# Performance work log

Measured on AMD Instinct MI355X. Metric: run time of the kernel, lower is better.

## Reference

```python
import jax, jax.numpy as jnp
import numpy as np


def setup_inputs() -> dict:
    key = jax.random.key(0)
    k1, k2, k3, k4 = jax.random.split(key, 4)
    B, S, H, P = 8, 2048, 1024, 4096
    hidden_states = jax.random.normal(k1, (B, S, H), dtype=jnp.float32)
    pairs = jax.random.randint(k2, (B, P, 2), 0, S, dtype=jnp.int64)
    # classifier params: Linear(2H -> H), Linear(H -> 2). Stored as (in, out).
    W1 = jax.random.normal(k3, (2 * H, H), dtype=jnp.float32) * (1.0 / np.sqrt(2 * H))
    b1 = jnp.zeros((H,), dtype=jnp.float32)
    W2 = jax.random.normal(k4, (H, 2), dtype=jnp.float32) * (1.0 / np.sqrt(H))
    b2 = jnp.zeros((2,), dtype=jnp.float32)
    return {"hidden_states": hidden_states, "pairs": pairs,
            "W1": W1, "b1": b1, "W2": W2, "b2": b2}


def reference(hidden_states, pairs, W1, b1, W2, b2):
    # Gather pair embeddings: (B, P, H) each.
    emb1 = jnp.take_along_axis(hidden_states, pairs[:, :, 0:1], axis=1)
    emb2 = jnp.take_along_axis(hidden_states, pairs[:, :, 1:2], axis=1)
    pair_emb = jnp.concatenate([emb1, emb2], axis=-1)  # (B, P, 2H)
    h = jnp.einsum('bpi,ih->bph', pair_emb, W1) + b1
    h = jax.nn.gelu(h, approximate=False)  # torch nn.GELU default is exact erf
    # Dropout is identity at inference.
    logits = jnp.einsum('bph,ho->bpo', h, W2) + b2  # (B, P, 2)
    return logits
```

## Files before the change

### kernel.cpp

```cpp
#include <hip/hip_runtime.h>
#include <hip/hip_bf16.h>

#define B_  8
#define S_  2048
#define H_  1024
#define P_  4096
#define K_  2048
#define M_  32768

typedef unsigned short u16;
using bf16x8 = __attribute__((ext_vector_type(8))) short;
using f32x4  = __attribute__((ext_vector_type(4))) float;

__device__ inline u16 f2bf(float f) {
  union { float f; unsigned u; } c; c.f = f;
  unsigned u = c.u;
  unsigned r = (u + 0x7fffu + ((u >> 16) & 1u)) >> 16;
  return (u16)r;
}

__global__ void cvt_hidden_k(const float4* __restrict__ src,
                             ushort4* __restrict__ dst, int n4) {
  int i = blockIdx.x * blockDim.x + threadIdx.x;
  int stride = gridDim.x * blockDim.x;
  for (; i < n4; i += stride) {
    float4 v = src[i];
    ushort4 o;
    o.x = f2bf(v.x); o.y = f2bf(v.y); o.z = f2bf(v.z); o.w = f2bf(v.w);
    dst[i] = o;
  }
}

__global__ void transp_w1_k(const float* __restrict__ w1, u16* __restrict__ w1t) {
  __shared__ float tile[32][33];
  int n0 = blockIdx.x * 32;
  int k0 = blockIdx.y * 32;
  int tx = threadIdx.x;
  int ty = threadIdx.y;
#pragma unroll
  for (int i = 0; i < 32; i += 8)
    tile[ty + i][tx] = w1[(size_t)(k0 + ty + i) * H_ + n0 + tx];
  __syncthreads();
#pragma unroll
  for (int i = 0; i < 32; i += 8)
    w1t[(size_t)(n0 + ty + i) * K_ + k0 + tx] = f2bf(tile[tx][ty + i]);
}

__global__ __launch_bounds__(512, 2) void gemm_k(
    const u16*  __restrict__ hidB,
    const u16*  __restrict__ w1t,
    const int*  __restrict__ pairs,
    const float* __restrict__ b1,
    const float2* __restrict__ w2,
    float*      __restrict__ part)
{
  __shared__ u16 ldsA[2][256 * 64];
  __shared__ u16 ldsB[2][256 * 64];

  int orig = blockIdx.x;
  int bid = (orig & 7) * (512 >> 3) + (orig >> 3);
  int nt = bid & 3;
  int mt = bid >> 2;
  int n0 = nt * 256;
  int m0 = mt * 256;
  int bI = m0 >> 12;
  int pp = m0 & 4095;

  int t = threadIdx.x;
  int w = t >> 6;
  int l = t & 63;
  int lr = l & 15;
  int lj = l >> 4;
  int wr = w >> 2;
  int wn = w & 3;

  int2 sv[4];
#pragma unroll
  for (int it = 0; it < 4; ++it) {
    int r = it * 64 + w * 8 + (l >> 3);
    sv[it] = ((const int2*)pairs)[bI * P_ + pp + r];
  }

  const u16* hidBase = hidB + ((size_t)bI << 21);

  f32x4 acc[8][4];
#pragma unroll
  for (int i = 0; i < 8; ++i)
#pragma unroll
    for (int j = 0; j < 4; ++j)
      acc[i][j] = (f32x4){0.f, 0.f, 0.f, 0.f};

  auto STAGE = [&](int buf, int kt) {
    int k0 = kt * 64;
    int kcol = k0 & 1023;
    int half = k0 >> 10;
#pragma unroll
    for (int it = 0; it < 4; ++it) {
      int r  = it * 64 + w * 8 + (l >> 3);
      int gs = (l & 7) ^ (r & 7);
      int s  = half ? sv[it].y : sv[it].x;
      __builtin_amdgcn_global_load_lds(
          (const __attribute__((address_space(1))) void*)
              (hidBase + (((size_t)s) << 10) + kcol + gs * 8),
          (__attribute__((address_space(3))) void*)&ldsA[buf][(it * 64 + w * 8) * 64],
          16, 0, 0);
      __builtin_amdgcn_global_load_lds(
          (const __attribute__((address_space(1))) void*)
              (w1t + ((size_t)(n0 + r)) * K_ + k0 + gs * 8),
          (__attribute__((address_space(3))) void*)&ldsB[buf][(it * 64 + w * 8) * 64],
          16, 0, 0);
    }
  };

  STAGE(0, 0);
  __syncthreads();

  int cur = 0;
  for (int kt = 0; kt < K_ / 64; ++kt) {
    if (kt < K_ / 64 - 1) STAGE(cur ^ 1, kt + 1);

#pragma unroll
    for (int ks = 0; ks < 2; ++ks) {
      bf16x8 af[8], bv[4];
      int gw = ks * 4 + lj;
#pragma unroll
      for (int mi = 0; mi < 8; ++mi) {
        int row = wr * 128 + mi * 16 + lr;
        af[mi] = *(const bf16x8*)&ldsA[cur][row * 64 + ((gw ^ (row & 7)) * 8)];
      }
#pragma unroll
      for (int ni = 0; ni < 4; ++ni) {
        int row = wn * 64 + ni * 16 + lr;
        bv[ni] = *(const bf16x8*)&ldsB[cur][row * 64 + ((gw ^ (row & 7)) * 8)];
      }
#pragma unroll
      for (int mi = 0; mi < 8; ++mi)
#pragma unroll
        for (int ni = 0; ni < 4; ++ni)
          acc[mi][ni] = __builtin_amdgcn_mfma_f32_16x16x32_bf16(
              af[mi], bv[ni], acc[mi][ni], 0, 0, 0);
    }
    __syncthreads();
    cur ^= 1;
  }

  int q = nt * 4 + wn;
  float2* pOut = (float2*)part;
#pragma unroll
  for (int mi = 0; mi < 8; ++mi) {
    float s0[4] = {0.f, 0.f, 0.f, 0.f};
    float s1[4] = {0.f, 0.f, 0.f, 0.f};
#pragma unroll
    for (int ni = 0; ni < 4; ++ni) {
      int n = n0 + wn * 64 + ni * 16 + lr;
      float bb = b1[n];
      float2 wv = w2[n];
#pragma unroll
      for (int j = 0; j < 4; ++j) {
        float x = acc[mi][ni][j] + bb;
        float g = 0.5f * x * (1.0f + erff(x * 0.70710678118654752f));
        s0[j] += g * wv.x;
        s1[j] += g * wv.y;
      }
    }
#pragma unroll
    for (int off = 1; off < 16; off <<= 1) {
#pragma unroll
      for (int j = 0; j < 4; ++j) {
        s0[j] += __shfl_xor(s0[j], off, 64);
        s1[j] += __shfl_xor(s1[j], off, 64);
      }
    }
    if (lr == 0) {
#pragma unroll
      for (int j = 0; j < 4; ++j) {
        int m = m0 + wr * 128 + mi * 16 + lj * 4 + j;
        pOut[((size_t)q << 15) + m] = make_float2(s0[j], s1[j]);
      }
    }
  }
}

__global__ void reduce_k(const float2* __restrict__ part,
                         const float* __restrict__ b2,
                         float2* __restrict__ out) {
  int m = blockIdx.x * blockDim.x + threadIdx.x;
  if (m >= M_) return;
  float a0 = b2[0], a1 = b2[1];
#pragma unroll
  for (int q = 0; q < 16; ++q) {
    float2 v = part[((size_t)q << 15) + m];
    a0 += v.x; a1 += v.y;
  }
  out[m] = make_float2(a0, a1);
}

extern "C" void kernel_launch(void* const* d_in, const int* in_sizes, int n_in,
                              void* d_out, int out_size, void* d_ws, size_t ws_size,
                              hipStream_t stream) {
  const float* hidden = (const float*)d_in[0];
  const int*   pairs  = (const int*)d_in[1];
  const float* W1     = (const float*)d_in[2];
  const float* b1     = (const float*)d_in[3];
  const float* W2     = (const float*)d_in[4];
  const float* b2     = (const float*)d_in[5];
  float* out = (float*)d_out;

  u16* hidB = (u16*)d_ws;
  u16* w1t  = hidB + (size_t)B_ * S_ * H_;
  float* part = (float*)(w1t + (size_t)H_ * K_);

  int n4 = (B_ * S_ * H_) / 4;
  cvt_hidden_k<<<4096, 256, 0, stream>>>((const float4*)hidden, (ushort4*)hidB, n4);
  transp_w1_k<<<dim3(H_ / 32, K_ / 32), dim3(32, 8), 0, stream>>>(W1, w1t);
  gemm_k<<<(M_ / 256) * (H_ / 256), 512, 0, stream>>>(
      hidB, w1t, pairs, b1, (const float2*)W2, part);
  reduce_k<<<(M_ + 255) / 256, 256, 0, stream>>>(
      (const float2*)part, b2, (float2*)out);
}
```

Baseline: 200.3 us.

## Deepen GEMM K-pipeline to four stages with explicit vmcnt waits and setprio

Restructures the GEMM main loop from a double-buffered 64-wide K tile into a four-buffer, 32-wide K tile pipeline with three stages in flight. It uses manual s_waitcnt vmcnt counters and raw s_barrier instead of __syncthreads, and raises wave priority around the MFMA block. The aim is to hide global-to-LDS load latency behind compute and cut barrier overhead. The cost is twice as many loop iterations and barriers, plus fragile hand-counted waits that must exactly match the outstanding loads.

```diff
diff --git a/kernel.cpp b/kernel.cpp
--- a/kernel.cpp
+++ b/kernel.cpp
@@ -7,10 +7,14 @@
 #define P_  4096
 #define K_  2048
 #define M_  32768
+#define NKT 64
 
 typedef unsigned short u16;
 using bf16x8 = __attribute__((ext_vector_type(8))) short;
 using f32x4  = __attribute__((ext_vector_type(4))) float;
+
+#define AS1 __attribute__((address_space(1)))
+#define AS3 __attribute__((address_space(3)))
 
 __device__ inline u16 f2bf(float f) {
   union { float f; unsigned u; } c; c.f = f;
@@ -54,8 +58,8 @@
     const float2* __restrict__ w2,
     float*      __restrict__ part)
 {
-  __shared__ u16 ldsA[2][256 * 64];
-  __shared__ u16 ldsB[2][256 * 64];
+  __shared__ u16 ldsA[4][256 * 32];
+  __shared__ u16 ldsB[4][256 * 32];
 
   int orig = blockIdx.x;
   int bid = (orig & 7) * (512 >> 3) + (orig >> 3);
@@ -74,12 +78,12 @@
   int wr = w >> 2;
   int wn = w & 3;
 
-  int2 sv[4];
-#pragma unroll
-  for (int it = 0; it < 4; ++it) {
-    int r = it * 64 + w * 8 + (l >> 3);
-    sv[it] = ((const int2*)pairs)[bI * P_ + pp + r];
-  }
+  int r0 = w * 16 + (l >> 2);
+  int r1 = 128 + r0;
+  int g0 = (l & 3) ^ (r0 & 3);
+
+  int2 sv0 = ((const int2*)pairs)[bI * P_ + pp + r0];
+  int2 sv1 = ((const int2*)pairs)[bI * P_ + pp + r1];
 
   const u16* hidBase = hidB + ((size_t)bI << 21);
 
@@ -91,58 +95,64 @@
       acc[i][j] = (f32x4){0.f, 0.f, 0.f, 0.f};
 
   auto STAGE = [&](int buf, int kt) {
-    int k0 = kt * 64;
+    int k0 = kt * 32;
     int kcol = k0 & 1023;
     int half = k0 >> 10;
-#pragma unroll
-    for (int it = 0; it < 4; ++it) {
-      int r  = it * 64 + w * 8 + (l >> 3);
-      int gs = (l & 7) ^ (r & 7);
-      int s  = half ? sv[it].y : sv[it].x;
-      __builtin_amdgcn_global_load_lds(
-          (const __attribute__((address_space(1))) void*)
-              (hidBase + (((size_t)s) << 10) + kcol + gs * 8),
-          (__attribute__((address_space(3))) void*)&ldsA[buf][(it * 64 + w * 8) * 64],
-          16, 0, 0);
-      __builtin_amdgcn_global_load_lds(
-          (const __attribute__((address_space(1))) void*)
-              (w1t + ((size_t)(n0 + r)) * K_ + k0 + gs * 8),
-          (__attribute__((address_space(3))) void*)&ldsB[buf][(it * 64 + w * 8) * 64],
-          16, 0, 0);
-    }
+    int sA0 = half ? sv0.y : sv0.x;
+    int sA1 = half ? sv1.y : sv1.x;
+    __builtin_amdgcn_global_load_lds(
+        (const AS1 void*)(hidBase + (((size_t)sA0) << 10) + kcol + g0 * 8),
+        (AS3 void*)&ldsA[buf][w * 512 + l * 8], 16, 0, 0);
+    __builtin_amdgcn_global_load_lds(
+        (const AS1 void*)(hidBase + (((size_t)sA1) << 10) + kcol + g0 * 8),
+        (AS3 void*)&ldsA[buf][4096 + w * 512 + l * 8], 16, 0, 0);
+    __builtin_amdgcn_global_load_lds(
+        (const AS1 void*)(w1t + (size_t)(n0 + r0) * K_ + k0 + g0 * 8),
+        (AS3 void*)&ldsB[buf][w * 512 + l * 8], 16, 0, 0);
+    __builtin_amdgcn_global_load_lds(
+        (const AS1 void*)(w1t + (size_t)(n0 + r1) * K_ + k0 + g0 * 8),
+        (AS3 void*)&ldsB[buf][4096 + w * 512 + l * 8], 16, 0, 0);
   };
 
-  STAGE(0, 0);
-  __syncthreads();
-
-  int cur = 0;
-  for (int kt = 0; kt < K_ / 64; ++kt) {
-    if (kt < K_ / 64 - 1) STAGE(cur ^ 1, kt + 1);
-
-#pragma unroll
-    for (int ks = 0; ks < 2; ++ks) {
-      bf16x8 af[8], bv[4];
-      int gw = ks * 4 + lj;
-#pragma unroll
-      for (int mi = 0; mi < 8; ++mi) {
-        int row = wr * 128 + mi * 16 + lr;
-        af[mi] = *(const bf16x8*)&ldsA[cur][row * 64 + ((gw ^ (row & 7)) * 8)];
-      }
-#pragma unroll
-      for (int ni = 0; ni < 4; ++ni) {
-        int row = wn * 64 + ni * 16 + lr;
-        bv[ni] = *(const bf16x8*)&ldsB[cur][row * 64 + ((gw ^ (row & 7)) * 8)];
-      }
-#pragma unroll
-      for (int mi = 0; mi < 8; ++mi)
-#pragma unroll
-        for (int ni = 0; ni < 4; ++ni)
-          acc[mi][ni] = __builtin_amdgcn_mfma_f32_16x16x32_bf16(
-              af[mi], bv[ni], acc[mi][ni], 0, 0, 0);
-    }
-    __syncthreads();
-    cur ^= 1;
-  }
+#define PHASE(KT, DOSTAGE, WAITOP)                                            \
+  {                                                                           \
+    const int buf_ = (KT) & 3;                                                \
+    bf16x8 af[8], bv[4];                                                      \
+    _Pragma("unroll")                                                         \
+    for (int mi = 0; mi < 8; ++mi) {                                          \
+      int row = wr * 128 + mi * 16 + lr;                                      \
+      af[mi] = *(const bf16x8*)&ldsA[buf_][row * 32 + ((lj ^ (row & 3)) * 8)];\
+    }                                                                         \
+    _Pragma("unroll")                                                         \
+    for (int ni = 0; ni < 4; ++ni) {                                          \
+      int row = wn * 64 + ni * 16 + lr;                                       \
+      bv[ni] = *(const bf16x8*)&ldsB[buf_][row * 32 + ((lj ^ (row & 3)) * 8)];\
+    }                                                                         \
+    if (DOSTAGE) STAGE((KT + 3) & 3, (KT) + 3);                               \
+    WAITOP;                                                                   \
+    __builtin_amdgcn_s_barrier();                                             \
+    __builtin_amdgcn_s_setprio(1);                                            \
+    _Pragma("unroll")                                                         \
+    for (int mi = 0; mi < 8; ++mi)                                            \
+      _Pragma("unroll")                                                       \
+      for (int ni = 0; ni < 4; ++ni)                                          \
+        acc[mi][ni] = __builtin_amdgcn_mfma_f32_16x16x32_bf16(                \
+            af[mi], bv[ni], acc[mi][ni], 0, 0, 0);                            \
+    __builtin_amdgcn_s_setprio(0);                                            \
+    __builtin_amdgcn_s_barrier();                                             \
+    asm volatile("" ::: "memory");                                            \
+  }
+
+  STAGE(0, 0); STAGE(1, 1); STAGE(2, 2);
+  asm volatile("s_waitcnt vmcnt(8)" ::: "memory");
+  __builtin_amdgcn_s_barrier();
+
+  for (int kt = 0; kt < NKT - 3; ++kt)
+    PHASE(kt, true, asm volatile("s_waitcnt vmcnt(8)" ::: "memory"));
+  PHASE(NKT - 3, false, asm volatile("s_waitcnt vmcnt(4)" ::: "memory"));
+  PHASE(NKT - 2, false, asm volatile("s_waitcnt vmcnt(0)" ::: "memory"));
+  PHASE(NKT - 1, false, );
+#undef PHASE
 
   int q = nt * 4 + wn;
   float2* pOut = (float2*)part;
```

Measured after the change: 189.2 us. 1.06x faster.

## Triple-buffer A tiles in LDS and load B fragments directly to registers

Applied to the files above, without the earlier changes.

The GEMM mainloop moves from a double-buffered LDS scheme for both operands to a three-slot LDS ring that holds only the gathered A rows, prefetched two tiles ahead. W1t fragments are now read straight from global memory into registers, one tile ahead and ping-ponged between two register sets. MFMA groups are wrapped in s_setprio to favour the math waves. This cuts LDS traffic and barrier stalls, but adds register pressure and relies on an explicit vmcnt(0) wait each tile, which also waits on the direct B loads.

```diff
diff --git a/kernel.cpp b/kernel.cpp
--- a/kernel.cpp
+++ b/kernel.cpp
@@ -7,10 +7,14 @@
 #define P_  4096
 #define K_  2048
 #define M_  32768
+#define NT_ 32
 
 typedef unsigned short u16;
 using bf16x8 = __attribute__((ext_vector_type(8))) short;
 using f32x4  = __attribute__((ext_vector_type(4))) float;
+
+#define AS1 __attribute__((address_space(1)))
+#define AS3 __attribute__((address_space(3)))
 
 __device__ inline u16 f2bf(float f) {
   union { float f; unsigned u; } c; c.f = f;
@@ -54,11 +58,10 @@
     const float2* __restrict__ w2,
     float*      __restrict__ part)
 {
-  __shared__ u16 ldsA[2][256 * 64];
-  __shared__ u16 ldsB[2][256 * 64];
+  __shared__ u16 lds[3 * 16384];
 
   int orig = blockIdx.x;
-  int bid = (orig & 7) * (512 >> 3) + (orig >> 3);
+  int bid = (orig & 7) * 64 + (orig >> 3);
   int nt = bid & 3;
   int mt = bid >> 2;
   int n0 = nt * 256;
@@ -74,14 +77,15 @@
   int wr = w >> 2;
   int wn = w & 3;
 
+  int gsrc = (l & 7) ^ ((l >> 3) & 7);
+
   int2 sv[4];
 #pragma unroll
-  for (int it = 0; it < 4; ++it) {
-    int r = it * 64 + w * 8 + (l >> 3);
-    sv[it] = ((const int2*)pairs)[bI * P_ + pp + r];
-  }
+  for (int i = 0; i < 4; ++i)
+    sv[i] = ((const int2*)pairs)[bI * P_ + pp + w * 32 + i * 8 + (l >> 3)];
 
   const u16* hidBase = hidB + ((size_t)bI << 21);
+  const u16* bRowBase = w1t + (size_t)(n0 + wn * 64 + lr) * K_;
 
   f32x4 acc[8][4];
 #pragma unroll
@@ -90,59 +94,75 @@
     for (int j = 0; j < 4; ++j)
       acc[i][j] = (f32x4){0.f, 0.f, 0.f, 0.f};
 
-  auto STAGE = [&](int buf, int kt) {
-    int k0 = kt * 64;
+  auto STAGE = [&](int tile) {
+    if (tile >= NT_) return;
+    unsigned reg = (unsigned)(tile % 3) * 16384u;
+    int k0 = tile * 64;
     int kcol = k0 & 1023;
     int half = k0 >> 10;
 #pragma unroll
-    for (int it = 0; it < 4; ++it) {
-      int r  = it * 64 + w * 8 + (l >> 3);
-      int gs = (l & 7) ^ (r & 7);
-      int s  = half ? sv[it].y : sv[it].x;
+    for (int i = 0; i < 4; ++i) {
+      int s = half ? sv[i].y : sv[i].x;
       __builtin_amdgcn_global_load_lds(
-          (const __attribute__((address_space(1))) void*)
-              (hidBase + (((size_t)s) << 10) + kcol + gs * 8),
-          (__attribute__((address_space(3))) void*)&ldsA[buf][(it * 64 + w * 8) * 64],
+          (const AS1 void*)(hidBase + (((size_t)s) << 10) + kcol + gsrc * 8),
+          (AS3 void*)&lds[reg + (unsigned)(w * 32 + i * 8) * 64u + (unsigned)l * 8u],
           16, 0, 0);
-      __builtin_amdgcn_global_load_lds(
-          (const __attribute__((address_space(1))) void*)
-              (w1t + ((size_t)(n0 + r)) * K_ + k0 + gs * 8),
-          (__attribute__((address_space(3))) void*)&ldsB[buf][(it * 64 + w * 8) * 64],
-          16, 0, 0);
     }
   };
 
-  STAGE(0, 0);
-  __syncthreads();
-
-  int cur = 0;
-  for (int kt = 0; kt < K_ / 64; ++kt) {
-    if (kt < K_ / 64 - 1) STAGE(cur ^ 1, kt + 1);
-
-#pragma unroll
-    for (int ks = 0; ks < 2; ++ks) {
-      bf16x8 af[8], bv[4];
-      int gw = ks * 4 + lj;
-#pragma unroll
-      for (int mi = 0; mi < 8; ++mi) {
-        int row = wr * 128 + mi * 16 + lr;
-        af[mi] = *(const bf16x8*)&ldsA[cur][row * 64 + ((gw ^ (row & 7)) * 8)];
-      }
-#pragma unroll
-      for (int ni = 0; ni < 4; ++ni) {
-        int row = wn * 64 + ni * 16 + lr;
-        bv[ni] = *(const bf16x8*)&ldsB[cur][row * 64 + ((gw ^ (row & 7)) * 8)];
-      }
-#pragma unroll
-      for (int mi = 0; mi < 8; ++mi)
-#pragma unroll
-        for (int ni = 0; ni < 4; ++ni)
-          acc[mi][ni] = __builtin_amdgcn_mfma_f32_16x16x32_bf16(
-              af[mi], bv[ni], acc[mi][ni], 0, 0, 0);
-    }
-    __syncthreads();
-    cur ^= 1;
-  }
+#define LOADB(BV, TB)                                                         \
+  {                                                                           \
+    int tb_ = (TB) < NT_ ? (TB) : NT_ - 1;                                    \
+    int kb_ = tb_ * 64;                                                       \
+    _Pragma("unroll")                                                         \
+    for (int ks = 0; ks < 2; ++ks)                                            \
+      _Pragma("unroll")                                                       \
+      for (int ni = 0; ni < 4; ++ni)                                          \
+        BV[ks][ni] = *(const bf16x8*)(bRowBase + (size_t)ni * 16 * K_ +       \
+                                      kb_ + ks * 32 + lj * 8);                \
+  }
+
+#define TILE(TI, BVU, BVN)                                                    \
+  {                                                                           \
+    const int ti_ = (TI);                                                     \
+    asm volatile("s_waitcnt vmcnt(0)" ::: "memory");                          \
+    __builtin_amdgcn_s_barrier();                                             \
+    STAGE(ti_ + 2);                                                           \
+    LOADB(BVN, ti_ + 1);                                                      \
+    unsigned reg_ = (unsigned)(ti_ % 3) * 16384u;                             \
+    _Pragma("unroll")                                                         \
+    for (int ks = 0; ks < 2; ++ks) {                                          \
+      _Pragma("unroll")                                                       \
+      for (int MH = 0; MH < 2; ++MH) {                                        \
+        bf16x8 af[4];                                                         \
+        _Pragma("unroll")                                                     \
+        for (int mi = 0; mi < 4; ++mi)                                        \
+          af[mi] = *(const bf16x8*)&lds[reg_ +                                \
+              (unsigned)(wr * 128 + MH * 64 + mi * 16 + lr) * 64u +           \
+              (unsigned)(((ks * 4 + lj) ^ (lr & 7)) * 8)];                    \
+        __builtin_amdgcn_s_setprio(1);                                        \
+        _Pragma("unroll")                                                     \
+        for (int mi = 0; mi < 4; ++mi)                                        \
+          _Pragma("unroll")                                                   \
+          for (int ni = 0; ni < 4; ++ni)                                      \
+            acc[MH * 4 + mi][ni] = __builtin_amdgcn_mfma_f32_16x16x32_bf16(   \
+                af[mi], BVU[ks][ni], acc[MH * 4 + mi][ni], 0, 0, 0);          \
+        __builtin_amdgcn_s_setprio(0);                                        \
+      }                                                                       \
+    }                                                                         \
+  }
+
+  bf16x8 bvA[2][4], bvB[2][4];
+
+  STAGE(0); STAGE(1);
+  LOADB(bvA, 0);
+
+  for (int u = 0; u < NT_ / 2; ++u) {
+    TILE(2 * u,     bvA, bvB);
+    TILE(2 * u + 1, bvB, bvA);
+  }
+#undef TILE
+#undef LOADB
 
   int q = nt * 4 + wn;
   float2* pOut = (float2*)part;
```

Result: slower. 236.1 us (+17.8%).

## Restructure GEMM main loop into quadrant-staged 8-wave ping-pong pipeline

Applied to the files above, without the earlier changes.

Replaces the simple double-buffered K loop with a finer-grained schedule. Each 64-wide K tile is split into A/B half-tiles loaded separately into a unified LDS buffer, and the MFMA work is split into four quadrants interleaved with the next tile's global->LDS loads. It uses explicit vmcnt/lgkmcnt waits, raw barriers and s_setprio to overlap memory with compute. The warp-to-output mapping changes (rows are interleaved across the two half-tiles), which adds synchronization complexity and the risk of subtle wait-count errors.

```diff
diff --git a/kernel.cpp b/kernel.cpp
--- a/kernel.cpp
+++ b/kernel.cpp
@@ -11,6 +11,9 @@
 typedef unsigned short u16;
 using bf16x8 = __attribute__((ext_vector_type(8))) short;
 using f32x4  = __attribute__((ext_vector_type(4))) float;
+
+#define AS1 __attribute__((address_space(1)))
+#define AS3 __attribute__((address_space(3)))
 
 __device__ inline u16 f2bf(float f) {
   union { float f; unsigned u; } c; c.f = f;
@@ -54,11 +57,10 @@
     const float2* __restrict__ w2,
     float*      __restrict__ part)
 {
-  __shared__ u16 ldsA[2][256 * 64];
-  __shared__ u16 ldsB[2][256 * 64];
+  __shared__ u16 lds[65536];
 
   int orig = blockIdx.x;
-  int bid = (orig & 7) * (512 >> 3) + (orig >> 3);
+  int bid = (orig & 7) * 64 + (orig >> 3);
   int nt = bid & 3;
   int mt = bid >> 2;
   int n0 = nt * 256;
@@ -74,12 +76,16 @@
   int wr = w >> 2;
   int wn = w & 3;
 
+  int rs   = w * 8 + (l >> 3);
+  int gsrc = (l & 7) ^ ((l >> 3) & 7);
+  unsigned xo[2];
+  xo[0] = (unsigned)(((lj) ^ (l & 7)) * 8);
+  xo[1] = (unsigned)(((4 + lj) ^ (l & 7)) * 8);
+
   int2 sv[4];
 #pragma unroll
-  for (int it = 0; it < 4; ++it) {
-    int r = it * 64 + w * 8 + (l >> 3);
-    sv[it] = ((const int2*)pairs)[bI * P_ + pp + r];
-  }
+  for (int i = 0; i < 4; ++i)
+    sv[i] = ((const int2*)pairs)[bI * P_ + pp + rs + 64 * i];
 
   const u16* hidBase = hidB + ((size_t)bI << 21);
 
@@ -90,59 +96,113 @@
     for (int j = 0; j < 4; ++j)
       acc[i][j] = (f32x4){0.f, 0.f, 0.f, 0.f};
 
-  auto STAGE = [&](int buf, int kt) {
-    int k0 = kt * 64;
+  auto STGA = [&](int d, int q, int T) {
+    int k0 = T * 64;
     int kcol = k0 & 1023;
     int half = k0 >> 10;
-#pragma unroll
-    for (int it = 0; it < 4; ++it) {
-      int r  = it * 64 + w * 8 + (l >> 3);
-      int gs = (l & 7) ^ (r & 7);
-      int s  = half ? sv[it].y : sv[it].x;
-      __builtin_amdgcn_global_load_lds(
-          (const __attribute__((address_space(1))) void*)
-              (hidBase + (((size_t)s) << 10) + kcol + gs * 8),
-          (__attribute__((address_space(3))) void*)&ldsA[buf][(it * 64 + w * 8) * 64],
-          16, 0, 0);
-      __builtin_amdgcn_global_load_lds(
-          (const __attribute__((address_space(1))) void*)
-              (w1t + ((size_t)(n0 + r)) * K_ + k0 + gs * 8),
-          (__attribute__((address_space(3))) void*)&ldsB[buf][(it * 64 + w * 8) * 64],
-          16, 0, 0);
-    }
+    int s0 = half ? sv[q].y     : sv[q].x;
+    int s1 = half ? sv[q + 2].y : sv[q + 2].x;
+    unsigned dst = (unsigned)d * 32768u + (unsigned)q * 8192u +
+                   (unsigned)(rs * 64 + (l & 7) * 8);
+    __builtin_amdgcn_global_load_lds(
+        (const AS1 void*)(hidBase + (((size_t)s0) << 10) + kcol + gsrc * 8),
+        (AS3 void*)&lds[dst], 16, 0, 0);
+    __builtin_amdgcn_global_load_lds(
+        (const AS1 void*)(hidBase + (((size_t)s1) << 10) + kcol + gsrc * 8),
+        (AS3 void*)&lds[dst + 4096], 16, 0, 0);
   };
-
-  STAGE(0, 0);
-  __syncthreads();
-
-  int cur = 0;
-  for (int kt = 0; kt < K_ / 64; ++kt) {
-    if (kt < K_ / 64 - 1) STAGE(cur ^ 1, kt + 1);
-
-#pragma unroll
-    for (int ks = 0; ks < 2; ++ks) {
-      bf16x8 af[8], bv[4];
-      int gw = ks * 4 + lj;
-#pragma unroll
-      for (int mi = 0; mi < 8; ++mi) {
-        int row = wr * 128 + mi * 16 + lr;
-        af[mi] = *(const bf16x8*)&ldsA[cur][row * 64 + ((gw ^ (row & 7)) * 8)];
-      }
-#pragma unroll
-      for (int ni = 0; ni < 4; ++ni) {
-        int row = wn * 64 + ni * 16 + lr;
-        bv[ni] = *(const bf16x8*)&ldsB[cur][row * 64 + ((gw ^ (row & 7)) * 8)];
-      }
-#pragma unroll
-      for (int mi = 0; mi < 8; ++mi)
-#pragma unroll
-        for (int ni = 0; ni < 4; ++ni)
-          acc[mi][ni] = __builtin_amdgcn_mfma_f32_16x16x32_bf16(
-              af[mi], bv[ni], acc[mi][ni], 0, 0, 0);
-    }
-    __syncthreads();
-    cur ^= 1;
-  }
+  auto STGB = [&](int d, int q, int T) {
+    int k0 = T * 64;
+    int c0 = ((rs >> 5) * 64) + q * 32 + (rs & 31);
+    int c1 = (((rs + 64) >> 5) * 64) + q * 32 + (rs & 31);
+    unsigned dst = (unsigned)d * 32768u + (unsigned)(2 + q) * 8192u +
+                   (unsigned)(rs * 64 + (l & 7) * 8);
+    __builtin_amdgcn_global_load_lds(
+        (const AS1 void*)(w1t + (size_t)(n0 + c0) * K_ + k0 + gsrc * 8),
+        (AS3 void*)&lds[dst], 16, 0, 0);
+    __builtin_amdgcn_global_load_lds(
+        (const AS1 void*)(w1t + (size_t)(n0 + c1) * K_ + k0 + gsrc * 8),
+        (AS3 void*)&lds[dst + 4096], 16, 0, 0);
+  };
+
+#define VM6 asm volatile("s_waitcnt vmcnt(6)" ::: "memory")
+#define VM0 asm volatile("s_waitcnt vmcnt(0)" ::: "memory")
+#define BAR __builtin_amdgcn_s_barrier()
+#define LK0 asm volatile("s_waitcnt lgkmcnt(0)" ::: "memory")
+#define LK8 asm volatile("s_waitcnt lgkmcnt(8)" ::: "memory")
+
+#define TILE(D, S1, S2, S3, S4, W4)                                           \
+  {                                                                           \
+    bf16x8 af[2][4], bva[2][2], bvb[2][2];                                    \
+                        \
+    _Pragma("unroll") for (int kk = 0; kk < 2; ++kk)                          \
+      _Pragma("unroll") for (int mi = 0; mi < 4; ++mi)                        \
+        af[kk][mi] = *(const bf16x8*)&lds[(D)*32768u +                        \
+            (unsigned)(wr*64 + mi*16 + lr)*64u + xo[kk]];                     \
+    _Pragma("unroll") for (int kk = 0; kk < 2; ++kk)                          \
+      _Pragma("unroll") for (int ni = 0; ni < 2; ++ni)                        \
+        bva[kk][ni] = *(const bf16x8*)&lds[(D)*32768u + 16384u +              \
+            (unsigned)(wn*32 + ni*16 + lr)*64u + xo[kk]];                     \
+    S1; LK8; BAR; LK0;                                                        \
+    __builtin_amdgcn_s_setprio(1);                                            \
+    _Pragma("unroll") for (int kk = 0; kk < 2; ++kk)                          \
+      _Pragma("unroll") for (int mi = 0; mi < 4; ++mi)                        \
+        _Pragma("unroll") for (int ni = 0; ni < 2; ++ni)                      \
+          acc[mi][ni] = __builtin_amdgcn_mfma_f32_16x16x32_bf16(              \
+              af[kk][mi], bva[kk][ni], acc[mi][ni], 0, 0, 0);                 \
+    __builtin_amdgcn_s_setprio(0); BAR;                                       \
+                                 \
+    _Pragma("unroll") for (int kk = 0; kk < 2; ++kk)                          \
+      _Pragma("unroll") for (int ni = 0; ni < 2; ++ni)                        \
+        bvb[kk][ni] = *(const bf16x8*)&lds[(D)*32768u + 24576u +              \
+            (unsigned)(wn*32 + ni*16 + lr)*64u + xo[kk]];                     \
+    S2; BAR; LK0;                                                             \
+    __builtin_amdgcn_s_setprio(1);                                            \
+    _Pragma("unroll") for (int kk = 0; kk < 2; ++kk)                          \
+      _Pragma("unroll") for (int mi = 0; mi < 4; ++mi)                        \
+        _Pragma("unroll") for (int ni = 0; ni < 2; ++ni)                      \
+          acc[mi][2 + ni] = __builtin_amdgcn_mfma_f32_16x16x32_bf16(          \
+              af[kk][mi], bvb[kk][ni], acc[mi][2 + ni], 0, 0, 0);             \
+    __builtin_amdgcn_s_setprio(0); BAR;                                       \
+                         \
+    _Pragma("unroll") for (int kk = 0; kk < 2; ++kk)                          \
+      _Pragma("unroll") for (int mi = 0; mi < 4; ++mi)                        \
+        af[kk][mi] = *(const bf16x8*)&lds[(D)*32768u + 8192u +                \
+            (unsigned)(wr*64 + mi*16 + lr)*64u + xo[kk]];                     \
+    S3; BAR; LK0;                                                             \
+    __builtin_amdgcn_s_setprio(1);                                            \
+    _Pragma("unroll") for (int kk = 0; kk < 2; ++kk)                          \
+      _Pragma("unroll") for (int mi = 0; mi < 4; ++mi)                        \
+        _Pragma("unroll") for (int ni = 0; ni < 2; ++ni)                      \
+          acc[4 + mi][2 + ni] = __builtin_amdgcn_mfma_f32_16x16x32_bf16(      \
+              af[kk][mi], bvb[kk][ni], acc[4 + mi][2 + ni], 0, 0, 0);         \
+    __builtin_amdgcn_s_setprio(0); BAR;                                       \
+          \
+    S4; W4; BAR;                                                              \
+    __builtin_amdgcn_s_setprio(1);                                            \
+    _Pragma("unroll") for (int kk = 0; kk < 2; ++kk)                          \
+      _Pragma("unroll") for (int mi = 0; mi < 4; ++mi)                        \
+        _Pragma("unroll") for (int ni = 0; ni < 2; ++ni)                      \
+          acc[4 + mi][ni] = __builtin_amdgcn_mfma_f32_16x16x32_bf16(          \
+              af[kk][mi], bva[kk][ni], acc[4 + mi][ni], 0, 0, 0);             \
+    __builtin_amdgcn_s_setprio(0); BAR;                                       \
+  }
+
+  STGA(0, 0, 0); STGB(0, 0, 0); STGB(0, 1, 0); STGA(0, 1, 0);
+  STGA(1, 0, 1); STGB(1, 0, 1); STGB(1, 1, 1);
+  VM6;
+  BAR;
+
+  for (int u = 0; u < 15; ++u) {
+    int T0 = 2 * u, T1 = 2 * u + 1;
+    TILE(0, STGA(1, 1, T0 + 1), STGA(0, 0, T0 + 2), STGB(0, 0, T0 + 2),
+            STGB(0, 1, T0 + 2), VM6);
+    TILE(1, STGA(0, 1, T1 + 1), STGA(1, 0, T1 + 2), STGB(1, 0, T1 + 2),
+            STGB(1, 1, T1 + 2), VM6);
+  }
+  TILE(0, STGA(1, 1, 31), , , , VM0);
+  TILE(1, , , , , );
+#undef TILE
 
   int q = nt * 4 + wn;
   float2* pOut = (float2*)part;
```

New measurement: 184.5 us. 1.09x faster.
